# Kernel tuning notes

Hardware: AMD Instinct MI355X
Metric: run time of the kernel (lower is better)

The kernel has to match this reference:

```python
import jax, jax.numpy as jnp
import numpy as np

# Izhikevich 'RS' (regular spiking) parameters; i_tonic filled to -1.5 in __init__
A, B, C, D = 0.02, 0.2, -65.0, 8.0
I_TONIC = -1.5
V_SPIKE = 30.0
RATE_DECAY = 0.95          # assumed EMA rate estimate in IzhikevichLayer
OSC_FREQ = 0.04
PC_TAU = 0.125             # assumed TwoCompColumn membrane leak per substep
PC_SUBSTEPS = 8


def setup_inputs() -> dict:
    key = jax.random.key(0)
    k1, k2, k3, k4 = jax.random.split(key, 4)
    return {
        "sensory_surprise": jax.random.uniform(k1, (1,), dtype=jnp.float32),
        "motor_mismatch": jax.random.uniform(k2, (1,), dtype=jnp.float32),
        "cerebellar_pe": jax.random.uniform(k3, (1,), dtype=jnp.float32),
        "prev_sensory": jnp.zeros((1,), jnp.float32),
        "prev_motor": jnp.zeros((1,), jnp.float32),
        "osc_phase": jnp.zeros((1,), jnp.float32),
        "v0": jnp.full((8,), C, jnp.float32),          # resting membrane potential
        "u0": jnp.full((8,), B * C, jnp.float32),      # resting recovery variable
        "rate0": jnp.zeros((8,), jnp.float32),
        "noise": jax.random.normal(k4, (10, 8), dtype=jnp.float32),
        "pc_m0": jnp.zeros((8,), jnp.float32),
    }


def reference(sensory_surprise, motor_mismatch, cerebellar_pe,
              prev_sensory, prev_motor, osc_phase,
              v0, u0, rate0, noise, pc_m0):
    s, m, cpe = sensory_surprise[0], motor_mismatch[0], cerebellar_pe[0]

    delta_sensory = jnp.abs(s - prev_sensory[0])
    sensory_error = jnp.minimum(1.0, delta_sensory + s * 0.3)
    delta_motor = jnp.abs(m - prev_motor[0])
    motor_error = jnp.minimum(1.0, delta_motor + m * 0.3)

    phase = osc_phase[0] + OSC_FREQ
    osc = 0.15 * jnp.sin(2.0 * jnp.pi * phase)

    raw_cf = sensory_error * 0.4 + motor_error * 0.4 + cpe * 0.2
    is_cs = raw_cf > 0.2
    climbing_fiber = jnp.where(is_cs,
                               jnp.minimum(1.0, raw_cf * 1.5),
                               jnp.maximum(0.0, raw_cf + osc))

    # input currents, 8 neurons (indices as in source)
    I = jnp.stack([
        sensory_error * 15.0,
        delta_sensory * 12.0,
        sensory_error * 8.0,
        osc * 5.0 + 2.0,
        motor_error * 15.0,
        delta_motor * 12.0,
        motor_error * 8.0,
        climbing_fiber * 10.0,
    ])

    def izh_step(carry, nz):
        v, u, r = carry
        Ii = I + nz * 0.3 + I_TONIC
        dv = 0.04 * v * v + 5.0 * v + 140.0 - u + Ii
        du = A * (B * v - u)
        v = v + dv
        u = u + du
        spike = v >= V_SPIKE
        v = jnp.where(spike, C, v)
        u = jnp.where(spike, u + D, u)
        r = RATE_DECAY * r + (1.0 - RATE_DECAY) * spike.astype(v.dtype)
        return (v, u, r), None

    (v, u, rate), _ = jax.lax.scan(izh_step, (v0, u0, rate0), noise)

    # TwoCompColumn: 2 channels x 4 neurons, 8 leaky-integrator substeps,
    # predictive-coding error = integrated (sensory - prediction) drive per channel
    sensory = jnp.stack([sensory_error, motor_error])      # [2]
    prediction = jnp.zeros((2,), sensory.dtype)
    drive = jnp.repeat(sensory - prediction, 4)            # [8]

    def pc_step(mem, _):
        mem = mem + PC_TAU * (drive - mem)
        return mem, None

    m_fin, _ = jax.lax.scan(pc_step, pc_m0, None, length=PC_SUBSTEPS)
    pe = m_fin.reshape(2, 4).mean(axis=1) - prediction     # [2]
    precision = 1.0 / (1.0 + pe * pe)                      # [2]
    free_energy = 0.5 * jnp.sum(precision * pe * pe)
    prediction_error = jnp.mean(jnp.abs(pe))

    return (sensory_error, motor_error, climbing_fiber,
            is_cs.astype(jnp.float32), prediction_error,
            precision.mean(), free_energy, rate.mean(), rate)
```

## Files before the change

kernel.cpp:

```cpp
#include <hip/hip_runtime.h>
#include <math.h>

#define A_P 0.02f
#define B_P 0.2f
#define C_P -65.0f
#define D_P 8.0f
#define I_TONIC -1.5f
#define V_SPIKE 30.0f
#define RATE_DECAY 0.95f
#define OSC_FREQ 0.04f
#define PC_TAU 0.125f
#define PC_SUBSTEPS 8
#define TWO_PI 6.28318530717958647692f

__global__ void __launch_bounds__(64)
SpikingInferiorOlive_kernel(const float* __restrict__ sensory_surprise,
                            const float* __restrict__ motor_mismatch,
                            const float* __restrict__ cerebellar_pe,
                            const float* __restrict__ prev_sensory,
                            const float* __restrict__ prev_motor,
                            const float* __restrict__ osc_phase,
                            const float* __restrict__ v0,
                            const float* __restrict__ u0,
                            const float* __restrict__ rate0,
                            const float* __restrict__ noise,
                            const float* __restrict__ pc_m0,
                            float* __restrict__ out)
{
    if (threadIdx.x != 0) return;

    const float s   = sensory_surprise[0];
    const float m   = motor_mismatch[0];
    const float cpe = cerebellar_pe[0];

    const float delta_sensory = fabsf(s - prev_sensory[0]);
    const float sensory_error = fminf(1.0f, delta_sensory + s * 0.3f);
    const float delta_motor   = fabsf(m - prev_motor[0]);
    const float motor_error   = fminf(1.0f, delta_motor + m * 0.3f);

    const float phase = osc_phase[0] + OSC_FREQ;
    const float osc   = 0.15f * sinf(TWO_PI * phase);

    const float raw_cf = sensory_error * 0.4f + motor_error * 0.4f + cpe * 0.2f;
    const bool  is_cs  = raw_cf > 0.2f;
    const float climbing_fiber = is_cs ? fminf(1.0f, raw_cf * 1.5f)
                                       : fmaxf(0.0f, raw_cf + osc);

    float I[8];
    I[0] = sensory_error * 15.0f;
    I[1] = delta_sensory * 12.0f;
    I[2] = sensory_error * 8.0f;
    I[3] = osc * 5.0f + 2.0f;
    I[4] = motor_error * 15.0f;
    I[5] = delta_motor * 12.0f;
    I[6] = motor_error * 8.0f;
    I[7] = climbing_fiber * 10.0f;

    float v[8], u[8], r[8];
#pragma unroll
    for (int i = 0; i < 8; ++i) { v[i] = v0[i]; u[i] = u0[i]; r[i] = rate0[i]; }

    const float one_minus_decay = 1.0f - RATE_DECAY;
#pragma unroll
    for (int t = 0; t < 10; ++t) {
#pragma unroll
        for (int i = 0; i < 8; ++i) {
            const float Ii = I[i] + noise[t * 8 + i] * 0.3f + I_TONIC;
            const float dv = 0.04f * v[i] * v[i] + 5.0f * v[i] + 140.0f - u[i] + Ii;
            const float du = A_P * (B_P * v[i] - u[i]);
            v[i] += dv;
            u[i] += du;
            const bool sp = (v[i] >= V_SPIKE);
            if (sp) { v[i] = C_P; u[i] += D_P; }
            r[i] = RATE_DECAY * r[i] + one_minus_decay * (sp ? 1.0f : 0.0f);
        }
    }

    float mem[8], drive[8];
#pragma unroll
    for (int i = 0; i < 8; ++i) {
        mem[i]   = pc_m0[i];
        drive[i] = (i < 4) ? sensory_error : motor_error;
    }
#pragma unroll
    for (int t = 0; t < PC_SUBSTEPS; ++t) {
#pragma unroll
        for (int i = 0; i < 8; ++i) mem[i] += PC_TAU * (drive[i] - mem[i]);
    }

    const float pe0 = (mem[0] + mem[1] + mem[2] + mem[3]) * 0.25f;
    const float pe1 = (mem[4] + mem[5] + mem[6] + mem[7]) * 0.25f;
    const float prec0 = 1.0f / (1.0f + pe0 * pe0);
    const float prec1 = 1.0f / (1.0f + pe1 * pe1);
    const float free_energy = 0.5f * (prec0 * pe0 * pe0 + prec1 * pe1 * pe1);
    const float prediction_error = 0.5f * (fabsf(pe0) + fabsf(pe1));

    float rate_mean = 0.0f;
#pragma unroll
    for (int i = 0; i < 8; ++i) rate_mean += r[i];
    rate_mean *= 0.125f;

    out[0] = sensory_error;
    out[1] = motor_error;
    out[2] = climbing_fiber;
    out[3] = is_cs ? 1.0f : 0.0f;
    out[4] = prediction_error;
    out[5] = (prec0 + prec1) * 0.5f;
    out[6] = free_energy;
    out[7] = rate_mean;
#pragma unroll
    for (int i = 0; i < 8; ++i) out[8 + i] = r[i];
}

extern "C" void kernel_launch(void* const* d_in, const int* in_sizes, int n_in,
                              void* d_out, int out_size, void* d_ws, size_t ws_size,
                              hipStream_t stream) {
    (void)in_sizes; (void)n_in; (void)d_ws; (void)ws_size; (void)out_size;
    SpikingInferiorOlive_kernel<<<1, 64, 0, stream>>>(
        (const float*)d_in[0],
        (const float*)d_in[1],
        (const float*)d_in[2],
        (const float*)d_in[3],
        (const float*)d_in[4],
        (const float*)d_in[5],
        (const float*)d_in[6],
        (const float*)d_in[7],
        (const float*)d_in[8],
        (const float*)d_in[9],
        (const float*)d_in[10],
        (float*)d_out);
}
```

Before: 9.584 us.

## Parallelize neurons across lanes, closed-form PC integrator, shuffle reductions

Maps each of the 8 neurons to its own lane instead of running all neurons serially on a single thread. The 8-step leaky integrator is replaced by one precomputed closed-form blend, and the means are computed with cross-lane xor shuffles. The first eight outputs are written as two float4 stores. This is meant to shorten the serial dependency chain in a launch-bound tiny kernel, at the cost of constant-folding the decay factor and relying on 16-byte alignment of the output.

```diff
diff --git a/kernel.cpp b/kernel.cpp
--- a/kernel.cpp
+++ b/kernel.cpp
@@ -9,9 +9,9 @@
 #define V_SPIKE 30.0f
 #define RATE_DECAY 0.95f
 #define OSC_FREQ 0.04f
-#define PC_TAU 0.125f
-#define PC_SUBSTEPS 8
 #define TWO_PI 6.28318530717958647692f
+#define PC_K 0.34360891580581665f
+#define PC_1MK 0.65639108419418335f
 
 __global__ void __launch_bounds__(64)
 SpikingInferiorOlive_kernel(const float* __restrict__ sensory_surprise,
@@ -27,7 +27,8 @@
                             const float* __restrict__ pc_m0,
                             float* __restrict__ out)
 {
-    if (threadIdx.x != 0) return;
+    const int lane = threadIdx.x;
+    const int n    = lane & 7;
 
     const float s   = sensory_surprise[0];
     const float m   = motor_mismatch[0];
@@ -46,70 +47,60 @@
     const float climbing_fiber = is_cs ? fminf(1.0f, raw_cf * 1.5f)
                                        : fmaxf(0.0f, raw_cf + osc);
 
-    float I[8];
-    I[0] = sensory_error * 15.0f;
-    I[1] = delta_sensory * 12.0f;
-    I[2] = sensory_error * 8.0f;
-    I[3] = osc * 5.0f + 2.0f;
-    I[4] = motor_error * 15.0f;
-    I[5] = delta_motor * 12.0f;
-    I[6] = motor_error * 8.0f;
-    I[7] = climbing_fiber * 10.0f;
+    float I =            sensory_error * 15.0f;
+    I = (n == 1) ? delta_sensory * 12.0f  : I;
+    I = (n == 2) ? sensory_error * 8.0f   : I;
+    I = (n == 3) ? osc * 5.0f + 2.0f      : I;
+    I = (n == 4) ? motor_error * 15.0f    : I;
+    I = (n == 5) ? delta_motor * 12.0f    : I;
+    I = (n == 6) ? motor_error * 8.0f     : I;
+    I = (n == 7) ? climbing_fiber * 10.0f : I;
 
-    float v[8], u[8], r[8];
-#pragma unroll
-    for (int i = 0; i < 8; ++i) { v[i] = v0[i]; u[i] = u0[i]; r[i] = rate0[i]; }
-
-    const float one_minus_decay = 1.0f - RATE_DECAY;
+    float v = v0[n], u = u0[n], r = rate0[n];
 #pragma unroll
     for (int t = 0; t < 10; ++t) {
-#pragma unroll
-        for (int i = 0; i < 8; ++i) {
-            const float Ii = I[i] + noise[t * 8 + i] * 0.3f + I_TONIC;
-            const float dv = 0.04f * v[i] * v[i] + 5.0f * v[i] + 140.0f - u[i] + Ii;
-            const float du = A_P * (B_P * v[i] - u[i]);
-            v[i] += dv;
-            u[i] += du;
-            const bool sp = (v[i] >= V_SPIKE);
-            if (sp) { v[i] = C_P; u[i] += D_P; }
-            r[i] = RATE_DECAY * r[i] + one_minus_decay * (sp ? 1.0f : 0.0f);
-        }
+        const float Ii = I + noise[t * 8 + n] * 0.3f + I_TONIC;
+        const float dv = 0.04f * v * v + 5.0f * v + 140.0f - u + Ii;
+        const float du = A_P * (B_P * v - u);
+        v = v + dv;
+        u = u + du;
+        const bool sp = (v >= V_SPIKE);
+        if (sp) { v = C_P; u += D_P; }
+        r = RATE_DECAY * r + (1.0f - RATE_DECAY) * (sp ? 1.0f : 0.0f);
     }
 
-    float mem[8], drive[8];
-#pragma unroll
-    for (int i = 0; i < 8; ++i) {
-        mem[i]   = pc_m0[i];
-        drive[i] = (i < 4) ? sensory_error : motor_error;
-    }
-#pragma unroll
-    for (int t = 0; t < PC_SUBSTEPS; ++t) {
-#pragma unroll
-        for (int i = 0; i < 8; ++i) mem[i] += PC_TAU * (drive[i] - mem[i]);
-    }
+    const float drive = (n < 4) ? sensory_error : motor_error;
+    const float mem   = PC_K * pc_m0[n] + PC_1MK * drive;
 
-    const float pe0 = (mem[0] + mem[1] + mem[2] + mem[3]) * 0.25f;
-    const float pe1 = (mem[4] + mem[5] + mem[6] + mem[7]) * 0.25f;
+    float psum = mem;
+    psum += __shfl_xor(psum, 1);
+    psum += __shfl_xor(psum, 2);
+    const float pe_self  = psum * 0.25f;
+    const float pe_other = __shfl_xor(pe_self, 4);
+    const float pe0 = (n < 4) ? pe_self : pe_other;
+    const float pe1 = (n < 4) ? pe_other : pe_self;
+
     const float prec0 = 1.0f / (1.0f + pe0 * pe0);
     const float prec1 = 1.0f / (1.0f + pe1 * pe1);
-    const float free_energy = 0.5f * (prec0 * pe0 * pe0 + prec1 * pe1 * pe1);
+    const float free_energy      = 0.5f * (prec0 * pe0 * pe0 + prec1 * pe1 * pe1);
     const float prediction_error = 0.5f * (fabsf(pe0) + fabsf(pe1));
+    const float precision_mean   = 0.5f * (prec0 + prec1);
 
-    float rate_mean = 0.0f;
-#pragma unroll
-    for (int i = 0; i < 8; ++i) rate_mean += r[i];
-    rate_mean *= 0.125f;
+    float rsum = r;
+    rsum += __shfl_xor(rsum, 1);
+    rsum += __shfl_xor(rsum, 2);
+    rsum += __shfl_xor(rsum, 4);
+    const float rate_mean = rsum * 0.125f;
 
-    out[0] = sensory_error;
-    out[1] = motor_error;
-    out[2] = climbing_fiber;
-    out[3] = is_cs ? 1.0f : 0.0f;
-    out[4] = prediction_error;
-    out[5] = (prec0 + prec1) * 0.5f;
-    out[6] = free_energy;
-    out[7] = rate_mean;
-#pragma unroll
-    for (int i = 0; i < 8; ++i) out[8 + i] = r[i];
+    if (lane == 0) {
+        float4 o0 = make_float4(sensory_error, motor_error, climbing_fiber,
+                                is_cs ? 1.0f : 0.0f);
+        float4 o1 = make_float4(prediction_error, precision_mean,
+                                free_energy, rate_mean);
+        *reinterpret_cast<float4*>(out)     = o0;
+        *reinterpret_cast<float4*>(out + 4) = o1;
+    }
+    if (lane < 8) out[8 + lane] = r;
 }
 
 extern "C" void kernel_launch(void* const* d_in, const int* in_sizes, int n_in,
```

New measurement: 9.613 us. Within noise of the previous version (+0.3%).
